# Performance work log

Hardware: AMD Instinct MI355X
Metric: run time of the kernel (lower is better)

## Reference

```python
import jax, jax.numpy as jnp
import numpy as np

N, E = 50000, 800000
IN_DIM, HID, HEADS, OUT_DIM = 128, 64, 4, 40
NEG_SLOPE = 0.2


def setup_inputs() -> dict:
    key = jax.random.key(0)
    ks = jax.random.split(key, 12)
    x = jax.random.normal(ks[0], (N, IN_DIM), dtype=jnp.float32)
    edge_index = jax.random.randint(ks[1], (2, E), 0, N, dtype=jnp.int64)
    timesteps = jax.random.randint(ks[2], (N,), 0, 100, dtype=jnp.int64)
    s = 1.0 / np.sqrt(IN_DIM)
    W_proj = jax.random.uniform(ks[3], (IN_DIM, HID), jnp.float32, -s, s)
    b_proj = jnp.zeros((HID,), jnp.float32)
    time_emb = jax.random.normal(ks[4], (100, HID), dtype=jnp.float32)
    sg = 1.0 / np.sqrt(HID)
    W_gat = jax.random.uniform(ks[5], (HID, HEADS * HID), jnp.float32, -sg, sg)
    att_src = jax.random.uniform(ks[6], (HEADS, HID), jnp.float32, -sg, sg)
    att_dst = jax.random.uniform(ks[7], (HEADS, HID), jnp.float32, -sg, sg)
    b_gat = jnp.zeros((HEADS * HID,), jnp.float32)
    sc = 1.0 / np.sqrt(HEADS * HID)
    W_cls = jax.random.uniform(ks[8], (HEADS * HID, OUT_DIM), jnp.float32, -sc, sc)
    b_cls = jnp.zeros((OUT_DIM,), jnp.float32)
    return {"x": x, "edge_index": edge_index, "timesteps": timesteps,
            "W_proj": W_proj, "b_proj": b_proj, "time_emb": time_emb,
            "W_gat": W_gat, "att_src": att_src, "att_dst": att_dst, "b_gat": b_gat,
            "W_cls": W_cls, "b_cls": b_cls}


def reference(x, edge_index, timesteps, W_proj, b_proj, time_emb,
              W_gat, att_src, att_dst, b_gat, W_cls, b_cls):
    n = x.shape[0]
    # feature projection + ReLU + time embedding
    h0 = jax.nn.relu(x @ W_proj + b_proj) + time_emb[timesteps]  # [N, HID]
    # --- GATConv (PyG semantics, add_self_loops=True, concat heads) ---
    h = (h0 @ W_gat).reshape(n, HEADS, HID)              # [N, H, C]
    a_src = jnp.einsum('nhc,hc->nh', h, att_src)         # [N, H]
    a_dst = jnp.einsum('nhc,hc->nh', h, att_dst)
    loops = jnp.arange(n, dtype=edge_index.dtype)
    src = jnp.concatenate([edge_index[0], loops])        # [E+N]
    dst = jnp.concatenate([edge_index[1], loops])
    e = jax.nn.leaky_relu(a_src[src] + a_dst[dst], NEG_SLOPE)  # [E+N, H]
    # segment softmax over incoming edges per destination node
    m = jax.ops.segment_max(e, dst, num_segments=n)      # [N, H]
    p = jnp.exp(e - m[dst])
    denom = jax.ops.segment_sum(p, dst, num_segments=n)  # [N, H]
    alpha = p / (denom[dst] + 1e-16)                     # [E+N, H]
    msg = alpha[:, :, None] * h[src]                     # [E+N, H, C]
    agg = jax.ops.segment_sum(msg, dst, num_segments=n)  # [N, H, C]
    gat_out = agg.reshape(n, HEADS * HID) + b_gat
    # ReLU + (dropout is identity in eval) + classifier
    return jax.nn.relu(gat_out) @ W_cls + b_cls          # [N, OUT_DIM]
```

## Files before the change

kernel.cpp:

```cpp
#include <hip/hip_runtime.h>
#include <hip/hip_fp16.h>

#define IN_DIM 128
#define HID 64
#define HEADS 4
#define OUT_DIM 40
#define CAP 64
#define NEG 0.2f
#define PA_EPB 4096
#define BKT_SH 9
#define BKT_CAP 10240
#define GPAD 264
#define HGP 72

__device__ __forceinline__ float lrelu(float v) { return v > 0.f ? v : NEG * v; }

union HU { float2 f2; __half2 h2[2]; };
union HU2 { float4 f4; __half2 h2[4]; };

typedef _Float16 f16x8 __attribute__((ext_vector_type(8)));
typedef float f32x4 __attribute__((ext_vector_type(4)));
union FU { float4 f4; f16x8 v; };

__global__ __launch_bounds__(256) void partA_kernel(
    const int* __restrict__ ei, int E, int nbkt, int paBlocks,
    int* __restrict__ cnt, unsigned int* __restrict__ ebuf,
    const float* __restrict__ Wg, const float* __restrict__ attS,
    const float* __restrict__ attD, const float* __restrict__ Wc,
    const float* __restrict__ Wp,
    float* __restrict__ aSf, float* __restrict__ aDf,
    __half* __restrict__ WgT, __half* __restrict__ WcTg,
    __half* __restrict__ WpT, __half* __restrict__ BsdT)
{
    if (blockIdx.x >= paBlocks) {
        int gid = (blockIdx.x - paBlocks) * 256 + threadIdx.x;
        if (gid < 256) {
            int k = gid >> 2, hd = gid & 3;
            const float* wr = Wg + k * 256 + hd * 64;
            const float* as = attS + hd * 64;
            const float* ad = attD + hd * 64;
            float ss = 0.f, dd = 0.f;
            for (int c = 0; c < 64; ++c) { float w = wr[c]; ss += w * as[c]; dd += w * ad[c]; }
            aSf[k * 4 + hd] = ss;
            aDf[k * 4 + hd] = dd;
        } else if (gid < 256 + 256 * HID) {
            int i = gid - 256;
            int o = i >> 6, k = i & 63;
            WgT[i] = __float2half(Wg[k * 256 + o]);
        } else if (gid < 256 + 256 * HID + OUT_DIM * 256) {
            int i = gid - 256 - 256 * HID;
            int o = i >> 8, k = i & 255;
            WcTg[i] = __float2half(Wc[k * OUT_DIM + o]);
        } else if (gid < 26880 + HID * IN_DIM) {
            int i = gid - 26880;
            int o = i >> 7, k = i & 127;
            WpT[i] = __float2half(Wp[k * HID + o]);
        } else if (gid < 26880 + HID * IN_DIM + 16 * HID) {
            int i = gid - 26880 - HID * IN_DIM;
            int n2 = i >> 6, k = i & 63;
            float v = 0.f;
            if (n2 < 8) {
                int hd = n2 & 3;
                const float* wr = Wg + k * 256 + hd * 64;
                const float* av = (n2 < 4) ? (attS + hd * 64) : (attD + hd * 64);
                for (int c = 0; c < 64; ++c) v += wr[c] * av[c];
            }
            BsdT[i] = __float2half(v);
        }
        return;
    }

    __shared__ int localCnt[128];
    __shared__ int baseArr[128];
    for (int i = threadIdx.x; i < nbkt; i += 256) localCnt[i] = 0;
    __syncthreads();

    const int e0 = blockIdx.x * PA_EPB + threadIdx.x;
    unsigned short l[16];
#pragma unroll
    for (int j = 0; j < 16; ++j) {
        int e = e0 + j * 256;
        if (e < E) {
            int d = ei[E + e];
            l[j] = (unsigned short)atomicAdd(&localCnt[d >> BKT_SH], 1);
        }
    }
    __syncthreads();
    for (int i = threadIdx.x; i < nbkt; i += 256)
        baseArr[i] = atomicAdd(&cnt[i], localCnt[i]);
    __syncthreads();
#pragma unroll
    for (int j = 0; j < 16; ++j) {
        int e = e0 + j * 256;
        if (e < E) {
            int s = ei[e];
            int d = ei[E + e];
            int b = d >> BKT_SH;
            int off = baseArr[b] + (int)l[j];
            if (off < BKT_CAP)
                ebuf[(size_t)b * BKT_CAP + off] =
                    ((unsigned)(d & ((1 << BKT_SH) - 1)) << 16) | (unsigned)s;
        }
    }
}

__global__ __launch_bounds__(256) void partBproj_kernel(
    const unsigned int* __restrict__ ebuf, const int* __restrict__ cnt,
    int* __restrict__ deg, unsigned short* __restrict__ csr, int nbkt,
    const float* __restrict__ x, const __half* __restrict__ WpT,
    const float* __restrict__ bp, const float* __restrict__ temb,
    const int* __restrict__ ts, const __half* __restrict__ BsdT,
    __half* __restrict__ h0h, float* __restrict__ aS, float* __restrict__ aD, int N)
{
    __shared__ __align__(16) char smem[32 * HGP * 2];

    if ((int)blockIdx.x < nbkt) {
        int* cntL = (int*)smem;
        const int b = blockIdx.x;
        for (int i = threadIdx.x; i < 512; i += 256) cntL[i] = 0;
        __syncthreads();

        int cb = cnt[b]; cb = cb < BKT_CAP ? cb : BKT_CAP;
        const unsigned int* eb = ebuf + (size_t)b * BKT_CAP;
        const int d0 = b << BKT_SH;
        for (int i = threadIdx.x; i < cb; i += 256) {
            unsigned v = eb[i];
            int dloc = v >> 16;
            int slot = atomicAdd(&cntL[dloc], 1);
            if (slot < CAP)
                csr[((size_t)(d0 + dloc) << 6) + slot] = (unsigned short)(v & 0xFFFFu);
        }
        __syncthreads();
        for (int i = threadIdx.x; i < 512; i += 256) {
            int d = d0 + i;
            if (d < N) deg[d] = cntL[i];
        }
        return;
    }

    __half* h0L = (__half*)smem;
    const int t = threadIdx.x;
    const int lane = t & 63, wq = t >> 6;
    const int m16 = lane & 15, quad = lane >> 4;
    const int mt = wq >> 1;
    const int ntb = (wq & 1) * 2;
    const int nodeBase = ((int)blockIdx.x - nbkt) * 32;

    f32x4 acc[2];
    acc[0] = (f32x4){0.f, 0.f, 0.f, 0.f};
    acc[1] = (f32x4){0.f, 0.f, 0.f, 0.f};

    {
        int n = nodeBase + mt * 16 + m16; n = n < N ? n : N - 1;
        const float* xr = x + (size_t)n * IN_DIM;
#pragma unroll
        for (int ks = 0; ks < 4; ++ks) {
            float4 xa = *(const float4*)(xr + ks * 32 + quad * 8);
            float4 xb = *(const float4*)(xr + ks * 32 + quad * 8 + 4);
            HU2 u;
            u.h2[0] = __floats2half2_rn(xa.x, xa.y);
            u.h2[1] = __floats2half2_rn(xa.z, xa.w);
            u.h2[2] = __floats2half2_rn(xb.x, xb.y);
            u.h2[3] = __floats2half2_rn(xb.z, xb.w);
            FU a; a.f4 = u.f4;
#pragma unroll
            for (int q = 0; q < 2; ++q) {
                int o = (ntb + q) * 16 + m16;
                FU b; b.f4 = *(const float4*)(WpT + o * IN_DIM + ks * 32 + quad * 8);
                acc[q] = __builtin_amdgcn_mfma_f32_16x16x32_f16(a.v, b.v, acc[q], 0, 0, 0);
            }
        }
    }

    {
        float bv[2];
#pragma unroll
        for (int q = 0; q < 2; ++q) bv[q] = bp[(ntb + q) * 16 + m16];
#pragma unroll
        for (int r = 0; r < 4; ++r) {
            int nloc = mt * 16 + quad * 4 + r;
            int n = nodeBase + nloc;
            if (n < N) {
                int tv = ts[n];
                const float* te = temb + (size_t)tv * HID;
#pragma unroll
                for (int q = 0; q < 2; ++q) {
                    int c = (ntb + q) * 16 + m16;
                    float v = fmaxf(acc[q][r] + bv[q], 0.f) + te[c];
                    h0L[nloc * HGP + c] = __float2half(v);
                }
            }
        }
    }
    __syncthreads();

    {
        int row = t >> 3, ch = (t & 7) * 8;
        int n = nodeBase + row;
        if (n < N)
            *(float4*)(h0h + (size_t)n * HID + ch) = *(const float4*)(h0L + row * HGP + ch);
    }

    if (wq < 2) {
        f32x4 acc2 = (f32x4){0.f, 0.f, 0.f, 0.f};
#pragma unroll
        for (int ks = 0; ks < 2; ++ks) {
            FU a; a.f4 = *(const float4*)(h0L + (wq * 16 + m16) * HGP + ks * 32 + quad * 8);
            FU b; b.f4 = *(const float4*)(BsdT + m16 * 64 + ks * 32 + quad * 8);
            acc2 = __builtin_amdgcn_mfma_f32_16x16x32_f16(a.v, b.v, acc2, 0, 0, 0);
        }
#pragma unroll
        for (int r = 0; r < 4; ++r) {
            int n = nodeBase + wq * 16 + quad * 4 + r;
            if (n < N) {
                if (m16 < 4)      aS[n * 4 + m16]       = acc2[r];
                else if (m16 < 8) aD[n * 4 + (m16 - 4)] = acc2[r];
            }
        }
    }
}

__global__ __launch_bounds__(256) void agg_kernel(
    const __half* __restrict__ h0h, const float* __restrict__ aS,
    const float* __restrict__ aD, const int* __restrict__ deg,
    const unsigned short* __restrict__ csr, __half* __restrict__ agg0h, int N)
{
    __shared__ float p_lds[4 * CAP * HEADS];
    __shared__ int   s_lds[4 * CAP];

    const int t = threadIdx.x;
    const int lane = t & 63, wq = t >> 6;
    const int n = blockIdx.x * 4 + wq;
    if (n >= N) return;
    const int hd16 = lane >> 4, li = lane & 15;

    const float adn = aD[n * 4 + hd16];
    const float es = lrelu(aS[n * 4 + hd16] + adn);

    int dn = deg[n]; dn = dn < CAP ? dn : CAP;
    const unsigned short* cs = csr + (size_t)n * CAP;
    float* pL = p_lds + wq * CAP * HEADS;
    int*   sL = s_lds + wq * CAP;

    float m = -1e30f;
    for (int i = li; i < dn; i += 16) {
        int src = cs[i];
        if (hd16 == 0) sL[i] = src << 7;
        float e = lrelu(aS[src * 4 + hd16] + adn);
        pL[i * HEADS + hd16] = e;
        m = fmaxf(m, e);
    }
#pragma unroll
    for (int off = 8; off > 0; off >>= 1)
        m = fmaxf(m, __shfl_xor(m, off));
    m = fmaxf(m, es);
    float mh[4], esh[4];
#pragma unroll
    for (int h = 0; h < 4; ++h) {
        mh[h]  = __shfl(m, h * 16);
        esh[h] = __shfl(es, h * 16);
    }

    float sp = 0.f;
    for (int idx = lane; idx < dn * 4; idx += 64) {
        float p = __expf(pL[idx] - mh[idx & 3]);
        pL[idx] = p;
        sp += p;
    }
#pragma unroll
    for (int off = 4; off < 64; off <<= 1)
        sp += __shfl_xor(sp, off);
    float pselfh[4], invh[4];
#pragma unroll
    for (int h = 0; h < 4; ++h) {
        float sh = __shfl(sp, h);
        pselfh[h] = __expf(esh[h] - mh[h]);
        invh[h] = 1.f / (sh + pselfh[h] + 1e-16f);
    }

    const int half = lane >> 5;
    const int ch2 = lane & 31;
    const char* hb = (const char*)h0h;
    const int laneByte = ch2 << 2;

    float2 acc[4];
    {
        float lo = 0.f, hi = 0.f;
        if (half == 0) {
            __half2 v2 = *(const __half2*)(hb + ((size_t)n << 7) + laneByte);
            float2 f = __half22float2(v2);
            lo = f.x; hi = f.y;
        }
#pragma unroll
        for (int h = 0; h < 4; ++h) {
            acc[h].x = pselfh[h] * lo;
            acc[h].y = pselfh[h] * hi;
        }
    }
    int i = 0;
    for (; i + 8 <= dn; i += 8) {
        int off0 = sL[i + 0 + half];
        int off1 = sL[i + 2 + half];
        int off2 = sL[i + 4 + half];
        int off3 = sL[i + 6 + half];
        __half2 v0 = *(const __half2*)(hb + off0 + laneByte);
        __half2 v1 = *(const __half2*)(hb + off1 + laneByte);
        __half2 v2 = *(const __half2*)(hb + off2 + laneByte);
        __half2 v3 = *(const __half2*)(hb + off3 + laneByte);
        float4 p0 = *(const float4*)(pL + (i + 0 + half) * 4);
        float4 p1 = *(const float4*)(pL + (i + 2 + half) * 4);
        float4 p2 = *(const float4*)(pL + (i + 4 + half) * 4);
        float4 p3 = *(const float4*)(pL + (i + 6 + half) * 4);
        float2 f;
        f = __half22float2(v0);
        acc[0].x += p0.x * f.x; acc[0].y += p0.x * f.y;
        acc[1].x += p0.y * f.x; acc[1].y += p0.y * f.y;
        acc[2].x += p0.z * f.x; acc[2].y += p0.z * f.y;
        acc[3].x += p0.w * f.x; acc[3].y += p0.w * f.y;
        f = __half22float2(v1);
        acc[0].x += p1.x * f.x; acc[0].y += p1.x * f.y;
        acc[1].x += p1.y * f.x; acc[1].y += p1.y * f.y;
        acc[2].x += p1.z * f.x; acc[2].y += p1.z * f.y;
        acc[3].x += p1.w * f.x; acc[3].y += p1.w * f.y;
        f = __half22float2(v2);
        acc[0].x += p2.x * f.x; acc[0].y += p2.x * f.y;
        acc[1].x += p2.y * f.x; acc[1].y += p2.y * f.y;
        acc[2].x += p2.z * f.x; acc[2].y += p2.z * f.y;
        acc[3].x += p2.w * f.x; acc[3].y += p2.w * f.y;
        f = __half22float2(v3);
        acc[0].x += p3.x * f.x; acc[0].y += p3.x * f.y;
        acc[1].x += p3.y * f.x; acc[1].y += p3.y * f.y;
        acc[2].x += p3.z * f.x; acc[2].y += p3.z * f.y;
        acc[3].x += p3.w * f.x; acc[3].y += p3.w * f.y;
    }
    for (; i + 2 <= dn; i += 2) {
        int off0 = sL[i + half];
        __half2 v0 = *(const __half2*)(hb + off0 + laneByte);
        float4 p0 = *(const float4*)(pL + (i + half) * 4);
        float2 f = __half22float2(v0);
        acc[0].x += p0.x * f.x; acc[0].y += p0.x * f.y;
        acc[1].x += p0.y * f.x; acc[1].y += p0.y * f.y;
        acc[2].x += p0.z * f.x; acc[2].y += p0.z * f.y;
        acc[3].x += p0.w * f.x; acc[3].y += p0.w * f.y;
    }
    if (i < dn && half == 0) {
        int off0 = sL[i];
        __half2 v0 = *(const __half2*)(hb + off0 + laneByte);
        float4 p0 = *(const float4*)(pL + i * 4);
        float2 f = __half22float2(v0);
        acc[0].x += p0.x * f.x; acc[0].y += p0.x * f.y;
        acc[1].x += p0.y * f.x; acc[1].y += p0.y * f.y;
        acc[2].x += p0.z * f.x; acc[2].y += p0.z * f.y;
        acc[3].x += p0.w * f.x; acc[3].y += p0.w * f.y;
    }
#pragma unroll
    for (int h = 0; h < 4; ++h) {
        acc[h].x += __shfl_xor(acc[h].x, 32);
        acc[h].y += __shfl_xor(acc[h].y, 32);
    }
    if (lane < 32) {
        __half2* dst = (__half2*)(agg0h + (size_t)n * 256);
#pragma unroll
        for (int h = 0; h < 4; ++h)
            dst[h * 32 + ch2] = __floats2half2_rn(acc[h].x * invh[h],
                                                  acc[h].y * invh[h]);
    }
}

__global__ __launch_bounds__(256) void gatcls_kernel(
    const __half* __restrict__ agg0h, const __half* __restrict__ WgT,
    const float* __restrict__ bg, const __half* __restrict__ WcTg,
    const float* __restrict__ bc, float* __restrict__ out, int N)
{
    __shared__ __half gtile[32 * GPAD];

    const int t = threadIdx.x;
    const int lane = t & 63, wq = t >> 6;
    const int m16 = lane & 15, quad = lane >> 4;
    const int nodeBase = blockIdx.x * 32;

    {
        const int h = wq;
        f32x4 acc[2][4];
#pragma unroll
        for (int mt = 0; mt < 2; ++mt)
#pragma unroll
            for (int nt = 0; nt < 4; ++nt)
                acc[mt][nt] = (f32x4){0.f, 0.f, 0.f, 0.f};

#pragma unroll
        for (int ks = 0; ks < 2; ++ks) {
            FU a[2], b[4];
#pragma unroll
            for (int mt = 0; mt < 2; ++mt) {
                int n = nodeBase + mt * 16 + m16; n = n < N ? n : N - 1;
                a[mt].f4 = *(const float4*)(agg0h + (size_t)n * 256 + h * 64 + ks * 32 + quad * 8);
            }
#pragma unroll
            for (int nt = 0; nt < 4; ++nt) {
                int o = h * 64 + nt * 16 + m16;
                b[nt].f4 = *(const float4*)(WgT + o * 64 + ks * 32 + quad * 8);
            }
#pragma unroll
            for (int mt = 0; mt < 2; ++mt)
#pragma unroll
                for (int nt = 0; nt < 4; ++nt)
                    acc[mt][nt] = __builtin_amdgcn_mfma_f32_16x16x32_f16(
                        a[mt].v, b[nt].v, acc[mt][nt], 0, 0, 0);
        }
#pragma unroll
        for (int nt = 0; nt < 4; ++nt) {
            int o = h * 64 + nt * 16 + m16;
            float bv = bg[o];
#pragma unroll
            for (int mt = 0; mt < 2; ++mt) {
#pragma unroll
                for (int r = 0; r < 4; ++r) {
                    int nloc = mt * 16 + quad * 4 + r;
                    gtile[nloc * GPAD + o] = __float2half(fmaxf(acc[mt][nt][r] + bv, 0.f));
                }
            }
        }
    }
    __syncthreads();

    {
        const int mt = wq >> 1;
        const int ntCount = (wq & 1) ? 1 : 2;
        const int ntBase = (wq & 1) ? 2 : 0;
        f32x4 acc2[2];
        acc2[0] = (f32x4){0.f, 0.f, 0.f, 0.f};
        acc2[1] = (f32x4){0.f, 0.f, 0.f, 0.f};
#pragma unroll
        for (int ks = 0; ks < 8; ++ks) {
            FU a; a.f4 = *(const float4*)(gtile + (mt * 16 + m16) * GPAD + ks * 32 + quad * 8);
            for (int q = 0; q < ntCount; ++q) {
                int o = (ntBase + q) * 16 + m16;
                int oc = o < OUT_DIM ? o : OUT_DIM - 1;
                FU b; b.f4 = *(const float4*)(WcTg + oc * 256 + ks * 32 + quad * 8);
                acc2[q] = __builtin_amdgcn_mfma_f32_16x16x32_f16(a.v, b.v, acc2[q], 0, 0, 0);
            }
        }
        for (int q = 0; q < ntCount; ++q) {
            int o = (ntBase + q) * 16 + m16;
            if (o < OUT_DIM) {
                float bv = bc[o];
#pragma unroll
                for (int r = 0; r < 4; ++r) {
                    int n = nodeBase + mt * 16 + quad * 4 + r;
                    if (n < N) out[(size_t)n * OUT_DIM + o] = acc2[q][r] + bv;
                }
            }
        }
    }
}

extern "C" void kernel_launch(void* const* d_in, const int* in_sizes, int n_in,
                              void* d_out, int out_size, void* d_ws, size_t ws_size,
                              hipStream_t stream) {
    const float* x    = (const float*)d_in[0];
    const int*   ei   = (const int*)d_in[1];
    const int*   ts   = (const int*)d_in[2];
    const float* Wp   = (const float*)d_in[3];
    const float* bp   = (const float*)d_in[4];
    const float* temb = (const float*)d_in[5];
    const float* Wg   = (const float*)d_in[6];
    const float* attS = (const float*)d_in[7];
    const float* attD = (const float*)d_in[8];
    const float* bg   = (const float*)d_in[9];
    const float* Wc   = (const float*)d_in[10];
    const float* bc   = (const float*)d_in[11];
    float* out = (float*)d_out;

    const int N = in_sizes[0] / IN_DIM;
    const int E = in_sizes[1] / 2;
    const int nbkt = (N + (1 << BKT_SH) - 1) >> BKT_SH;

    char* w = (char*)d_ws;
    __half*         h0h   = (__half*)w;         w += (size_t)N * HID * 2;
    __half*         agg0h = (__half*)w;         w += (size_t)N * 256 * 2;
    float*          aS    = (float*)w;          w += (size_t)N * HEADS * 4;
    float*          aD    = (float*)w;          w += (size_t)N * HEADS * 4;
    int*            deg   = (int*)w;            w += (size_t)N * 4;
    unsigned short* csr   = (unsigned short*)w; w += (size_t)N * CAP * 2;
    unsigned int*   ebuf  = (unsigned int*)w;   w += (size_t)nbkt * BKT_CAP * 4;
    int*            cnt   = (int*)w;            w += (size_t)nbkt * 4;
    float*          aSf   = (float*)w;          w += 256 * 4;
    float*          aDf   = (float*)w;          w += 256 * 4;
    __half*         WgT   = (__half*)w;         w += (size_t)256 * HID * 2;
    __half*         WcTg  = (__half*)w;         w += (size_t)OUT_DIM * 256 * 2;
    __half*         WpT   = (__half*)w;         w += (size_t)HID * IN_DIM * 2;
    __half*         BsdT  = (__half*)w;         w += (size_t)16 * HID * 2;

    const int paBlocks = (E + PA_EPB - 1) / PA_EPB;
    const int prepWork = 256 + 256 * HID + OUT_DIM * 256
                       + HID * IN_DIM + 16 * HID;
    const int prepBlocks = (prepWork + 255) / 256;
    const int projBlocks = (N + 31) / 32;

    hipMemsetAsync(cnt, 0, (size_t)nbkt * 4, stream);
    partA_kernel<<<paBlocks + prepBlocks, 256, 0, stream>>>(
        ei, E, nbkt, paBlocks, cnt, ebuf, Wg, attS, attD, Wc, Wp,
        aSf, aDf, WgT, WcTg, WpT, BsdT);
    partBproj_kernel<<<nbkt + projBlocks, 256, 0, stream>>>(
        ebuf, cnt, deg, csr, nbkt, x, WpT, bp, temb, ts, BsdT, h0h, aS, aD, N);
    agg_kernel<<<(N + 3) / 4, 256, 0, stream>>>(h0h, aS, aD, deg, csr, agg0h, N);
    gatcls_kernel<<<(N + 31) / 32, 256, 0, stream>>>(agg0h, WgT, bg, WcTg, bc, out, N);
}
```

Measured before the change: 198.6 us.

## Replace two-pass bucketed CSR build with direct global-atomic scatter

The two-level bucket sort (partA bucketing into ebuf, then per-bucket shared-memory slotting) is replaced by one pass in which each edge does a global atomicAdd on deg[dst] and writes its source straight into the fixed-capacity CSR row. Degree zeroing moves into the weight-prep kernel, which removes the memset and the unused aSf/aDf computation, and the CSR build now runs in the same launch as the projection. This drops one full read/write of the edge buffer and a launch, but uses many scattered global atomics on random destinations in place of shared-memory atomics.

```diff
diff --git a/kernel.cpp b/kernel.cpp
--- a/kernel.cpp
+++ b/kernel.cpp
@@ -7,9 +7,6 @@
 #define OUT_DIM 40
 #define CAP 64
 #define NEG 0.2f
-#define PA_EPB 4096
-#define BKT_SH 9
-#define BKT_CAP 10240
 #define GPAD 264
 #define HGP 72
 
@@ -22,129 +19,71 @@
 typedef float f32x4 __attribute__((ext_vector_type(4)));
 union FU { float4 f4; f16x8 v; };
 
-__global__ __launch_bounds__(256) void partA_kernel(
-    const int* __restrict__ ei, int E, int nbkt, int paBlocks,
-    int* __restrict__ cnt, unsigned int* __restrict__ ebuf,
+__global__ __launch_bounds__(256) void prep_kernel(
     const float* __restrict__ Wg, const float* __restrict__ attS,
     const float* __restrict__ attD, const float* __restrict__ Wc,
     const float* __restrict__ Wp,
-    float* __restrict__ aSf, float* __restrict__ aDf,
     __half* __restrict__ WgT, __half* __restrict__ WcTg,
-    __half* __restrict__ WpT, __half* __restrict__ BsdT)
+    __half* __restrict__ WpT, __half* __restrict__ BsdT,
+    int* __restrict__ deg, int N)
 {
-    if (blockIdx.x >= paBlocks) {
-        int gid = (blockIdx.x - paBlocks) * 256 + threadIdx.x;
-        if (gid < 256) {
-            int k = gid >> 2, hd = gid & 3;
+    int gid = blockIdx.x * 256 + threadIdx.x;
+    if (gid < 16384) {
+        int o = gid >> 6, k = gid & 63;
+        WgT[gid] = __float2half(Wg[k * 256 + o]);
+    } else if (gid < 26624) {
+        int i = gid - 16384;
+        int o = i >> 8, k = i & 255;
+        WcTg[i] = __float2half(Wc[k * OUT_DIM + o]);
+    } else if (gid < 34816) {
+        int i = gid - 26624;
+        int o = i >> 7, k = i & 127;
+        WpT[i] = __float2half(Wp[k * HID + o]);
+    } else if (gid < 35840) {
+        int i = gid - 34816;
+        int n2 = i >> 6, k = i & 63;
+        float v = 0.f;
+        if (n2 < 8) {
+            int hd = n2 & 3;
             const float* wr = Wg + k * 256 + hd * 64;
-            const float* as = attS + hd * 64;
-            const float* ad = attD + hd * 64;
-            float ss = 0.f, dd = 0.f;
-            for (int c = 0; c < 64; ++c) { float w = wr[c]; ss += w * as[c]; dd += w * ad[c]; }
-            aSf[k * 4 + hd] = ss;
-            aDf[k * 4 + hd] = dd;
-        } else if (gid < 256 + 256 * HID) {
-            int i = gid - 256;
-            int o = i >> 6, k = i & 63;
-            WgT[i] = __float2half(Wg[k * 256 + o]);
-        } else if (gid < 256 + 256 * HID + OUT_DIM * 256) {
-            int i = gid - 256 - 256 * HID;
-            int o = i >> 8, k = i & 255;
-            WcTg[i] = __float2half(Wc[k * OUT_DIM + o]);
-        } else if (gid < 26880 + HID * IN_DIM) {
-            int i = gid - 26880;
-            int o = i >> 7, k = i & 127;
-            WpT[i] = __float2half(Wp[k * HID + o]);
-        } else if (gid < 26880 + HID * IN_DIM + 16 * HID) {
-            int i = gid - 26880 - HID * IN_DIM;
-            int n2 = i >> 6, k = i & 63;
-            float v = 0.f;
-            if (n2 < 8) {
-                int hd = n2 & 3;
-                const float* wr = Wg + k * 256 + hd * 64;
-                const float* av = (n2 < 4) ? (attS + hd * 64) : (attD + hd * 64);
-                for (int c = 0; c < 64; ++c) v += wr[c] * av[c];
-            }
-            BsdT[i] = __float2half(v);
-        }
-        return;
-    }
-
-    __shared__ int localCnt[128];
-    __shared__ int baseArr[128];
-    for (int i = threadIdx.x; i < nbkt; i += 256) localCnt[i] = 0;
-    __syncthreads();
-
-    const int e0 = blockIdx.x * PA_EPB + threadIdx.x;
-    unsigned short l[16];
-#pragma unroll
-    for (int j = 0; j < 16; ++j) {
-        int e = e0 + j * 256;
-        if (e < E) {
-            int d = ei[E + e];
-            l[j] = (unsigned short)atomicAdd(&localCnt[d >> BKT_SH], 1);
-        }
-    }
-    __syncthreads();
-    for (int i = threadIdx.x; i < nbkt; i += 256)
-        baseArr[i] = atomicAdd(&cnt[i], localCnt[i]);
-    __syncthreads();
-#pragma unroll
-    for (int j = 0; j < 16; ++j) {
-        int e = e0 + j * 256;
-        if (e < E) {
-            int s = ei[e];
-            int d = ei[E + e];
-            int b = d >> BKT_SH;
-            int off = baseArr[b] + (int)l[j];
-            if (off < BKT_CAP)
-                ebuf[(size_t)b * BKT_CAP + off] =
-                    ((unsigned)(d & ((1 << BKT_SH) - 1)) << 16) | (unsigned)s;
-        }
+            const float* av = (n2 < 4) ? (attS + hd * 64) : (attD + hd * 64);
+            for (int c = 0; c < 64; ++c) v += wr[c] * av[c];
+        }
+        BsdT[i] = __float2half(v);
+    } else {
+        int d = gid - 35840;
+        if (d < N) deg[d] = 0;
     }
 }
 
-__global__ __launch_bounds__(256) void partBproj_kernel(
-    const unsigned int* __restrict__ ebuf, const int* __restrict__ cnt,
-    int* __restrict__ deg, unsigned short* __restrict__ csr, int nbkt,
+__global__ __launch_bounds__(256) void binproj_kernel(
+    const int* __restrict__ ei, int E, int nbin,
+    int* __restrict__ deg, unsigned short* __restrict__ csr,
     const float* __restrict__ x, const __half* __restrict__ WpT,
     const float* __restrict__ bp, const float* __restrict__ temb,
     const int* __restrict__ ts, const __half* __restrict__ BsdT,
     __half* __restrict__ h0h, float* __restrict__ aS, float* __restrict__ aD, int N)
 {
-    __shared__ __align__(16) char smem[32 * HGP * 2];
-
-    if ((int)blockIdx.x < nbkt) {
-        int* cntL = (int*)smem;
-        const int b = blockIdx.x;
-        for (int i = threadIdx.x; i < 512; i += 256) cntL[i] = 0;
-        __syncthreads();
-
-        int cb = cnt[b]; cb = cb < BKT_CAP ? cb : BKT_CAP;
-        const unsigned int* eb = ebuf + (size_t)b * BKT_CAP;
-        const int d0 = b << BKT_SH;
-        for (int i = threadIdx.x; i < cb; i += 256) {
-            unsigned v = eb[i];
-            int dloc = v >> 16;
-            int slot = atomicAdd(&cntL[dloc], 1);
+    __shared__ __align__(16) __half h0L[32 * HGP];
+
+    if ((int)blockIdx.x < nbin) {
+        int e = blockIdx.x * 256 + threadIdx.x;
+        if (e < E) {
+            int s = ei[e];
+            int d = ei[E + e];
+            int slot = atomicAdd(&deg[d], 1);
             if (slot < CAP)
-                csr[((size_t)(d0 + dloc) << 6) + slot] = (unsigned short)(v & 0xFFFFu);
-        }
-        __syncthreads();
-        for (int i = threadIdx.x; i < 512; i += 256) {
-            int d = d0 + i;
-            if (d < N) deg[d] = cntL[i];
+                csr[(size_t)d * CAP + slot] = (unsigned short)s;
         }
         return;
     }
 
-    __half* h0L = (__half*)smem;
     const int t = threadIdx.x;
     const int lane = t & 63, wq = t >> 6;
     const int m16 = lane & 15, quad = lane >> 4;
     const int mt = wq >> 1;
     const int ntb = (wq & 1) * 2;
-    const int nodeBase = ((int)blockIdx.x - nbkt) * 32;
+    const int nodeBase = ((int)blockIdx.x - nbin) * 32;
 
     f32x4 acc[2];
     acc[0] = (f32x4){0.f, 0.f, 0.f, 0.f};
@@ -474,7 +413,6 @@
 
     const int N = in_sizes[0] / IN_DIM;
     const int E = in_sizes[1] / 2;
-    const int nbkt = (N + (1 << BKT_SH) - 1) >> BKT_SH;
 
     char* w = (char*)d_ws;
     __half*         h0h   = (__half*)w;         w += (size_t)N * HID * 2;
@@ -483,27 +421,20 @@
     float*          aD    = (float*)w;          w += (size_t)N * HEADS * 4;
     int*            deg   = (int*)w;            w += (size_t)N * 4;
     unsigned short* csr   = (unsigned short*)w; w += (size_t)N * CAP * 2;
-    unsigned int*   ebuf  = (unsigned int*)w;   w += (size_t)nbkt * BKT_CAP * 4;
-    int*            cnt   = (int*)w;            w += (size_t)nbkt * 4;
-    float*          aSf   = (float*)w;          w += 256 * 4;
-    float*          aDf   = (float*)w;          w += 256 * 4;
     __half*         WgT   = (__half*)w;         w += (size_t)256 * HID * 2;
     __half*         WcTg  = (__half*)w;         w += (size_t)OUT_DIM * 256 * 2;
     __half*         WpT   = (__half*)w;         w += (size_t)HID * IN_DIM * 2;
     __half*         BsdT  = (__half*)w;         w += (size_t)16 * HID * 2;
 
-    const int paBlocks = (E + PA_EPB - 1) / PA_EPB;
-    const int prepWork = 256 + 256 * HID + OUT_DIM * 256
-                       + HID * IN_DIM + 16 * HID;
+    const int prepWork  = 35840 + N;
     const int prepBlocks = (prepWork + 255) / 256;
+    const int nbin      = (E + 255) / 256;
     const int projBlocks = (N + 31) / 32;
 
-    hipMemsetAsync(cnt, 0, (size_t)nbkt * 4, stream);
-    partA_kernel<<<paBlocks + prepBlocks, 256, 0, stream>>>(
-        ei, E, nbkt, paBlocks, cnt, ebuf, Wg, attS, attD, Wc, Wp,
-        aSf, aDf, WgT, WcTg, WpT, BsdT);
-    partBproj_kernel<<<nbkt + projBlocks, 256, 0, stream>>>(
-        ebuf, cnt, deg, csr, nbkt, x, WpT, bp, temb, ts, BsdT, h0h, aS, aD, N);
+    prep_kernel<<<prepBlocks, 256, 0, stream>>>(
+        Wg, attS, attD, Wc, Wp, WgT, WcTg, WpT, BsdT, deg, N);
+    binproj_kernel<<<nbin + projBlocks, 256, 0, stream>>>(
+        ei, E, nbin, deg, csr, x, WpT, bp, temb, ts, BsdT, h0h, aS, aD, N);
     agg_kernel<<<(N + 3) / 4, 256, 0, stream>>>(h0h, aS, aD, deg, csr, agg0h, N);
     gatcls_kernel<<<(N + 31) / 32, 256, 0, stream>>>(agg0h, WgT, bg, WcTg, bc, out, N);
 }
```

New measurement: 217.6 us. 1.1x slower.

## Fuse attention aggregation with GAT linear and classifier into one kernel

Applied to the files above, without the earlier changes.

Merges the aggregation kernel with the GAT-projection and classifier MFMA kernel. The per-node aggregated features now stay in LDS instead of making a round trip through a global fp16 buffer. Each 4-node block runs 16-row MFMA tiles with only 4 valid rows and reloads the full WgT and WcTg weights per block, which adds wasted matrix work and weight traffic. It also drops the unused aSf/aDf precompute and shrinks edges per partition block from 4096 to 1024 to launch more blocks.

```diff
diff --git a/kernel.cpp b/kernel.cpp
--- a/kernel.cpp
+++ b/kernel.cpp
@@ -7,10 +7,10 @@
 #define OUT_DIM 40
 #define CAP 64
 #define NEG 0.2f
-#define PA_EPB 4096
+#define PA_EPB 1024
 #define BKT_SH 9
 #define BKT_CAP 10240
-#define GPAD 264
+#define GP2 264
 #define HGP 72
 
 __device__ __forceinline__ float lrelu(float v) { return v > 0.f ? v : NEG * v; }
@@ -28,35 +28,24 @@
     const float* __restrict__ Wg, const float* __restrict__ attS,
     const float* __restrict__ attD, const float* __restrict__ Wc,
     const float* __restrict__ Wp,
-    float* __restrict__ aSf, float* __restrict__ aDf,
     __half* __restrict__ WgT, __half* __restrict__ WcTg,
     __half* __restrict__ WpT, __half* __restrict__ BsdT)
 {
     if (blockIdx.x >= paBlocks) {
         int gid = (blockIdx.x - paBlocks) * 256 + threadIdx.x;
-        if (gid < 256) {
-            int k = gid >> 2, hd = gid & 3;
-            const float* wr = Wg + k * 256 + hd * 64;
-            const float* as = attS + hd * 64;
-            const float* ad = attD + hd * 64;
-            float ss = 0.f, dd = 0.f;
-            for (int c = 0; c < 64; ++c) { float w = wr[c]; ss += w * as[c]; dd += w * ad[c]; }
-            aSf[k * 4 + hd] = ss;
-            aDf[k * 4 + hd] = dd;
-        } else if (gid < 256 + 256 * HID) {
-            int i = gid - 256;
-            int o = i >> 6, k = i & 63;
-            WgT[i] = __float2half(Wg[k * 256 + o]);
-        } else if (gid < 256 + 256 * HID + OUT_DIM * 256) {
-            int i = gid - 256 - 256 * HID;
+        if (gid < 16384) {
+            int o = gid >> 6, k = gid & 63;
+            WgT[gid] = __float2half(Wg[k * 256 + o]);
+        } else if (gid < 26624) {
+            int i = gid - 16384;
             int o = i >> 8, k = i & 255;
             WcTg[i] = __float2half(Wc[k * OUT_DIM + o]);
-        } else if (gid < 26880 + HID * IN_DIM) {
-            int i = gid - 26880;
+        } else if (gid < 34816) {
+            int i = gid - 26624;
             int o = i >> 7, k = i & 127;
             WpT[i] = __float2half(Wp[k * HID + o]);
-        } else if (gid < 26880 + HID * IN_DIM + 16 * HID) {
-            int i = gid - 26880 - HID * IN_DIM;
+        } else if (gid < 35840) {
+            int i = gid - 34816;
             int n2 = i >> 6, k = i & 63;
             float v = 0.f;
             if (n2 < 8) {
@@ -76,9 +65,9 @@
     __syncthreads();
 
     const int e0 = blockIdx.x * PA_EPB + threadIdx.x;
-    unsigned short l[16];
-#pragma unroll
-    for (int j = 0; j < 16; ++j) {
+    unsigned short l[4];
+#pragma unroll
+    for (int j = 0; j < 4; ++j) {
         int e = e0 + j * 256;
         if (e < E) {
             int d = ei[E + e];
@@ -90,7 +79,7 @@
         baseArr[i] = atomicAdd(&cnt[i], localCnt[i]);
     __syncthreads();
 #pragma unroll
-    for (int j = 0; j < 16; ++j) {
+    for (int j = 0; j < 4; ++j) {
         int e = e0 + j * 256;
         if (e < E) {
             int s = ei[e];
@@ -220,236 +209,206 @@
     }
 }
 
-__global__ __launch_bounds__(256) void agg_kernel(
+__global__ __launch_bounds__(256) void aggcls_kernel(
     const __half* __restrict__ h0h, const float* __restrict__ aS,
     const float* __restrict__ aD, const int* __restrict__ deg,
-    const unsigned short* __restrict__ csr, __half* __restrict__ agg0h, int N)
+    const unsigned short* __restrict__ csr,
+    const __half* __restrict__ WgT, const float* __restrict__ bg,
+    const __half* __restrict__ WcTg, const float* __restrict__ bc,
+    float* __restrict__ out, int N)
 {
-    __shared__ float p_lds[4 * CAP * HEADS];
-    __shared__ int   s_lds[4 * CAP];
+    __shared__ __half agg0L[16 * GP2];
+    __shared__ union {
+        struct { float p[4 * CAP * HEADS]; int s[4 * CAP]; } g;
+        __half gatL[16 * GP2];
+    } su;
 
     const int t = threadIdx.x;
     const int lane = t & 63, wq = t >> 6;
     const int n = blockIdx.x * 4 + wq;
-    if (n >= N) return;
     const int hd16 = lane >> 4, li = lane & 15;
-
-    const float adn = aD[n * 4 + hd16];
-    const float es = lrelu(aS[n * 4 + hd16] + adn);
-
-    int dn = deg[n]; dn = dn < CAP ? dn : CAP;
-    const unsigned short* cs = csr + (size_t)n * CAP;
-    float* pL = p_lds + wq * CAP * HEADS;
-    int*   sL = s_lds + wq * CAP;
-
-    float m = -1e30f;
-    for (int i = li; i < dn; i += 16) {
-        int src = cs[i];
-        if (hd16 == 0) sL[i] = src << 7;
-        float e = lrelu(aS[src * 4 + hd16] + adn);
-        pL[i * HEADS + hd16] = e;
-        m = fmaxf(m, e);
-    }
-#pragma unroll
-    for (int off = 8; off > 0; off >>= 1)
-        m = fmaxf(m, __shfl_xor(m, off));
-    m = fmaxf(m, es);
-    float mh[4], esh[4];
-#pragma unroll
-    for (int h = 0; h < 4; ++h) {
-        mh[h]  = __shfl(m, h * 16);
-        esh[h] = __shfl(es, h * 16);
-    }
-
-    float sp = 0.f;
-    for (int idx = lane; idx < dn * 4; idx += 64) {
-        float p = __expf(pL[idx] - mh[idx & 3]);
-        pL[idx] = p;
-        sp += p;
-    }
-#pragma unroll
-    for (int off = 4; off < 64; off <<= 1)
-        sp += __shfl_xor(sp, off);
-    float pselfh[4], invh[4];
-#pragma unroll
-    for (int h = 0; h < 4; ++h) {
-        float sh = __shfl(sp, h);
-        pselfh[h] = __expf(esh[h] - mh[h]);
-        invh[h] = 1.f / (sh + pselfh[h] + 1e-16f);
-    }
-
     const int half = lane >> 5;
     const int ch2 = lane & 31;
     const char* hb = (const char*)h0h;
     const int laneByte = ch2 << 2;
 
-    float2 acc[4];
-    {
-        float lo = 0.f, hi = 0.f;
-        if (half == 0) {
-            __half2 v2 = *(const __half2*)(hb + ((size_t)n << 7) + laneByte);
-            float2 f = __half22float2(v2);
-            lo = f.x; hi = f.y;
-        }
+    if (n < N) {
+        const float adn = aD[n * 4 + hd16];
+        const float es = lrelu(aS[n * 4 + hd16] + adn);
+
+        int dn = deg[n]; dn = dn < CAP ? dn : CAP;
+        const unsigned short* cs = csr + (size_t)n * CAP;
+        float* pL = su.g.p + wq * CAP * HEADS;
+        int*   sL = su.g.s + wq * CAP;
+
+        float m = -1e30f;
+        for (int i = li; i < dn; i += 16) {
+            int src = cs[i];
+            if (hd16 == 0) sL[i] = src << 7;
+            float e = lrelu(aS[src * 4 + hd16] + adn);
+            pL[i * HEADS + hd16] = e;
+            m = fmaxf(m, e);
+        }
+#pragma unroll
+        for (int off = 8; off > 0; off >>= 1)
+            m = fmaxf(m, __shfl_xor(m, off));
+        m = fmaxf(m, es);
+        float mh[4], esh[4];
 #pragma unroll
         for (int h = 0; h < 4; ++h) {
-            acc[h].x = pselfh[h] * lo;
-            acc[h].y = pselfh[h] * hi;
-        }
-    }
-    int i = 0;
-    for (; i + 8 <= dn; i += 8) {
-        int off0 = sL[i + 0 + half];
-        int off1 = sL[i + 2 + half];
-        int off2 = sL[i + 4 + half];
-        int off3 = sL[i + 6 + half];
-        __half2 v0 = *(const __half2*)(hb + off0 + laneByte);
-        __half2 v1 = *(const __half2*)(hb + off1 + laneByte);
-        __half2 v2 = *(const __half2*)(hb + off2 + laneByte);
-        __half2 v3 = *(const __half2*)(hb + off3 + laneByte);
-        float4 p0 = *(const float4*)(pL + (i + 0 + half) * 4);
-        float4 p1 = *(const float4*)(pL + (i + 2 + half) * 4);
-        float4 p2 = *(const float4*)(pL + (i + 4 + half) * 4);
-        float4 p3 = *(const float4*)(pL + (i + 6 + half) * 4);
-        float2 f;
-        f = __half22float2(v0);
-        acc[0].x += p0.x * f.x; acc[0].y += p0.x * f.y;
-        acc[1].x += p0.y * f.x; acc[1].y += p0.y * f.y;
-        acc[2].x += p0.z * f.x; acc[2].y += p0.z * f.y;
-        acc[3].x += p0.w * f.x; acc[3].y += p0.w * f.y;
-        f = __half22float2(v1);
-        acc[0].x += p1.x * f.x; acc[0].y += p1.x * f.y;
-        acc[1].x += p1.y * f.x; acc[1].y += p1.y * f.y;
-        acc[2].x += p1.z * f.x; acc[2].y += p1.z * f.y;
-        acc[3].x += p1.w * f.x; acc[3].y += p1.w * f.y;
-        f = __half22float2(v2);
-        acc[0].x += p2.x * f.x; acc[0].y += p2.x * f.y;
-        acc[1].x += p2.y * f.x; acc[1].y += p2.y * f.y;
-        acc[2].x += p2.z * f.x; acc[2].y += p2.z * f.y;
-        acc[3].x += p2.w * f.x; acc[3].y += p2.w * f.y;
-        f = __half22float2(v3);
-        acc[0].x += p3.x * f.x; acc[0].y += p3.x * f.y;
-        acc[1].x += p3.y * f.x; acc[1].y += p3.y * f.y;
-        acc[2].x += p3.z * f.x; acc[2].y += p3.z * f.y;
-        acc[3].x += p3.w * f.x; acc[3].y += p3.w * f.y;
-    }
-    for (; i + 2 <= dn; i += 2) {
-        int off0 = sL[i + half];
-        __half2 v0 = *(const __half2*)(hb + off0 + laneByte);
-        float4 p0 = *(const float4*)(pL + (i + half) * 4);
-        float2 f = __half22float2(v0);
-        acc[0].x += p0.x * f.x; acc[0].y += p0.x * f.y;
-        acc[1].x += p0.y * f.x; acc[1].y += p0.y * f.y;
-        acc[2].x += p0.z * f.x; acc[2].y += p0.z * f.y;
-        acc[3].x += p0.w * f.x; acc[3].y += p0.w * f.y;
-    }
-    if (i < dn && half == 0) {
-        int off0 = sL[i];
-        __half2 v0 = *(const __half2*)(hb + off0 + laneByte);
-        float4 p0 = *(const float4*)(pL + i * 4);
-        float2 f = __half22float2(v0);
-        acc[0].x += p0.x * f.x; acc[0].y += p0.x * f.y;
-        acc[1].x += p0.y * f.x; acc[1].y += p0.y * f.y;
-        acc[2].x += p0.z * f.x; acc[2].y += p0.z * f.y;
-        acc[3].x += p0.w * f.x; acc[3].y += p0.w * f.y;
-    }
-#pragma unroll
-    for (int h = 0; h < 4; ++h) {
-        acc[h].x += __shfl_xor(acc[h].x, 32);
-        acc[h].y += __shfl_xor(acc[h].y, 32);
-    }
-    if (lane < 32) {
-        __half2* dst = (__half2*)(agg0h + (size_t)n * 256);
-#pragma unroll
-        for (int h = 0; h < 4; ++h)
-            dst[h * 32 + ch2] = __floats2half2_rn(acc[h].x * invh[h],
-                                                  acc[h].y * invh[h]);
-    }
-}
-
-__global__ __launch_bounds__(256) void gatcls_kernel(
-    const __half* __restrict__ agg0h, const __half* __restrict__ WgT,
-    const float* __restrict__ bg, const __half* __restrict__ WcTg,
-    const float* __restrict__ bc, float* __restrict__ out, int N)
-{
-    __shared__ __half gtile[32 * GPAD];
-
-    const int t = threadIdx.x;
-    const int lane = t & 63, wq = t >> 6;
+            mh[h]  = __shfl(m, h * 16);
+            esh[h] = __shfl(es, h * 16);
+        }
+
+        float sp = 0.f;
+        for (int idx = lane; idx < dn * 4; idx += 64) {
+            float p = __expf(pL[idx] - mh[idx & 3]);
+            pL[idx] = p;
+            sp += p;
+        }
+#pragma unroll
+        for (int off = 4; off < 64; off <<= 1)
+            sp += __shfl_xor(sp, off);
+        float pselfh[4], invh[4];
+#pragma unroll
+        for (int h = 0; h < 4; ++h) {
+            float sh = __shfl(sp, h);
+            pselfh[h] = __expf(esh[h] - mh[h]);
+            invh[h] = 1.f / (sh + pselfh[h] + 1e-16f);
+        }
+
+        float2 acc[4];
+        {
+            float lo = 0.f, hi = 0.f;
+            if (half == 0) {
+                __half2 v2 = *(const __half2*)(hb + ((size_t)n << 7) + laneByte);
+                float2 f = __half22float2(v2);
+                lo = f.x; hi = f.y;
+            }
+#pragma unroll
+            for (int h = 0; h < 4; ++h) {
+                acc[h].x = pselfh[h] * lo;
+                acc[h].y = pselfh[h] * hi;
+            }
+        }
+        int i = 0;
+        for (; i + 8 <= dn; i += 8) {
+            int off0 = sL[i + 0 + half];
+            int off1 = sL[i + 2 + half];
+            int off2 = sL[i + 4 + half];
+            int off3 = sL[i + 6 + half];
+            __half2 v0 = *(const __half2*)(hb + off0 + laneByte);
+            __half2 v1 = *(const __half2*)(hb + off1 + laneByte);
+            __half2 v2 = *(const __half2*)(hb + off2 + laneByte);
+            __half2 v3 = *(const __half2*)(hb + off3 + laneByte);
+            float4 p0 = *(const float4*)(pL + (i + 0 + half) * 4);
+            float4 p1 = *(const float4*)(pL + (i + 2 + half) * 4);
+            float4 p2 = *(const float4*)(pL + (i + 4 + half) * 4);
+            float4 p3 = *(const float4*)(pL + (i + 6 + half) * 4);
+            float2 f;
+            f = __half22float2(v0);
+            acc[0].x += p0.x * f.x; acc[0].y += p0.x * f.y;
+            acc[1].x += p0.y * f.x; acc[1].y += p0.y * f.y;
+            acc[2].x += p0.z * f.x; acc[2].y += p0.z * f.y;
+            acc[3].x += p0.w * f.x; acc[3].y += p0.w * f.y;
+            f = __half22float2(v1);
+            acc[0].x += p1.x * f.x; acc[0].y += p1.x * f.y;
+            acc[1].x += p1.y * f.x; acc[1].y += p1.y * f.y;
+            acc[2].x += p1.z * f.x; acc[2].y += p1.z * f.y;
+            acc[3].x += p1.w * f.x; acc[3].y += p1.w * f.y;
+            f = __half22float2(v2);
+            acc[0].x += p2.x * f.x; acc[0].y += p2.x * f.y;
+            acc[1].x += p2.y * f.x; acc[1].y += p2.y * f.y;
+            acc[2].x += p2.z * f.x; acc[2].y += p2.z * f.y;
+            acc[3].x += p2.w * f.x; acc[3].y += p2.w * f.y;
+            f = __half22float2(v3);
+            acc[0].x += p3.x * f.x; acc[0].y += p3.x * f.y;
+            acc[1].x += p3.y * f.x; acc[1].y += p3.y * f.y;
+            acc[2].x += p3.z * f.x; acc[2].y += p3.z * f.y;
+            acc[3].x += p3.w * f.x; acc[3].y += p3.w * f.y;
+        }
+        for (; i + 2 <= dn; i += 2) {
+            int off0 = sL[i + half];
+            __half2 v0 = *(const __half2*)(hb + off0 + laneByte);
+            float4 p0 = *(const float4*)(pL + (i + half) * 4);
+            float2 f = __half22float2(v0);
+            acc[0].x += p0.x * f.x; acc[0].y += p0.x * f.y;
+            acc[1].x += p0.y * f.x; acc[1].y += p0.y * f.y;
+            acc[2].x += p0.z * f.x; acc[2].y += p0.z * f.y;
+            acc[3].x += p0.w * f.x; acc[3].y += p0.w * f.y;
+        }
+        if (i < dn && half == 0) {
+            int off0 = sL[i];
+            __half2 v0 = *(const __half2*)(hb + off0 + laneByte);
+            float4 p0 = *(const float4*)(pL + i * 4);
+            float2 f = __half22float2(v0);
+            acc[0].x += p0.x * f.x; acc[0].y += p0.x * f.y;
+            acc[1].x += p0.y * f.x; acc[1].y += p0.y * f.y;
+            acc[2].x += p0.z * f.x; acc[2].y += p0.z * f.y;
+            acc[3].x += p0.w * f.x; acc[3].y += p0.w * f.y;
+        }
+#pragma unroll
+        for (int h = 0; h < 4; ++h) {
+            acc[h].x += __shfl_xor(acc[h].x, 32);
+            acc[h].y += __shfl_xor(acc[h].y, 32);
+        }
+        if (lane < 32) {
+            __half2* dst = (__half2*)(agg0L + wq * GP2);
+#pragma unroll
+            for (int h = 0; h < 4; ++h)
+                dst[h * 32 + ch2] = __floats2half2_rn(acc[h].x * invh[h],
+                                                      acc[h].y * invh[h]);
+        }
+    }
+    __syncthreads();
+
     const int m16 = lane & 15, quad = lane >> 4;
-    const int nodeBase = blockIdx.x * 32;
 
     {
         const int h = wq;
-        f32x4 acc[2][4];
-#pragma unroll
-        for (int mt = 0; mt < 2; ++mt)
-#pragma unroll
-            for (int nt = 0; nt < 4; ++nt)
-                acc[mt][nt] = (f32x4){0.f, 0.f, 0.f, 0.f};
-
+        f32x4 acc1[4];
+#pragma unroll
+        for (int nt = 0; nt < 4; ++nt)
+            acc1[nt] = (f32x4){0.f, 0.f, 0.f, 0.f};
 #pragma unroll
         for (int ks = 0; ks < 2; ++ks) {
-            FU a[2], b[4];
-#pragma unroll
-            for (int mt = 0; mt < 2; ++mt) {
-                int n = nodeBase + mt * 16 + m16; n = n < N ? n : N - 1;
-                a[mt].f4 = *(const float4*)(agg0h + (size_t)n * 256 + h * 64 + ks * 32 + quad * 8);
-            }
+            FU a; a.f4 = *(const float4*)(agg0L + m16 * GP2 + h * 64 + ks * 32 + quad * 8);
 #pragma unroll
             for (int nt = 0; nt < 4; ++nt) {
                 int o = h * 64 + nt * 16 + m16;
-                b[nt].f4 = *(const float4*)(WgT + o * 64 + ks * 32 + quad * 8);
-            }
-#pragma unroll
-            for (int mt = 0; mt < 2; ++mt)
-#pragma unroll
-                for (int nt = 0; nt < 4; ++nt)
-                    acc[mt][nt] = __builtin_amdgcn_mfma_f32_16x16x32_f16(
-                        a[mt].v, b[nt].v, acc[mt][nt], 0, 0, 0);
+                FU b; b.f4 = *(const float4*)(WgT + o * 64 + ks * 32 + quad * 8);
+                acc1[nt] = __builtin_amdgcn_mfma_f32_16x16x32_f16(a.v, b.v, acc1[nt], 0, 0, 0);
+            }
         }
 #pragma unroll
         for (int nt = 0; nt < 4; ++nt) {
             int o = h * 64 + nt * 16 + m16;
             float bv = bg[o];
 #pragma unroll
-            for (int mt = 0; mt < 2; ++mt) {
-#pragma unroll
-                for (int r = 0; r < 4; ++r) {
-                    int nloc = mt * 16 + quad * 4 + r;
-                    gtile[nloc * GPAD + o] = __float2half(fmaxf(acc[mt][nt][r] + bv, 0.f));
-                }
-            }
-        }
-    }
-    __syncthreads();
-
-    {
-        const int mt = wq >> 1;
-        const int ntCount = (wq & 1) ? 1 : 2;
-        const int ntBase = (wq & 1) ? 2 : 0;
-        f32x4 acc2[2];
-        acc2[0] = (f32x4){0.f, 0.f, 0.f, 0.f};
-        acc2[1] = (f32x4){0.f, 0.f, 0.f, 0.f};
+            for (int r = 0; r < 4; ++r) {
+                int row = quad * 4 + r;
+                su.gatL[row * GP2 + o] = __float2half(fmaxf(acc1[nt][r] + bv, 0.f));
+            }
+        }
+    }
+    __syncthreads();
+
+    if (wq < 3) {
+        f32x4 acc2 = (f32x4){0.f, 0.f, 0.f, 0.f};
+        int o = wq * 16 + m16;
+        int oc = o < OUT_DIM ? o : OUT_DIM - 1;
 #pragma unroll
         for (int ks = 0; ks < 8; ++ks) {
-            FU a; a.f4 = *(const float4*)(gtile + (mt * 16 + m16) * GPAD + ks * 32 + quad * 8);
-            for (int q = 0; q < ntCount; ++q) {
-                int o = (ntBase + q) * 16 + m16;
-                int oc = o < OUT_DIM ? o : OUT_DIM - 1;
-                FU b; b.f4 = *(const float4*)(WcTg + oc * 256 + ks * 32 + quad * 8);
-                acc2[q] = __builtin_amdgcn_mfma_f32_16x16x32_f16(a.v, b.v, acc2[q], 0, 0, 0);
-            }
-        }
-        for (int q = 0; q < ntCount; ++q) {
-            int o = (ntBase + q) * 16 + m16;
-            if (o < OUT_DIM) {
-                float bv = bc[o];
-#pragma unroll
-                for (int r = 0; r < 4; ++r) {
-                    int n = nodeBase + mt * 16 + quad * 4 + r;
-                    if (n < N) out[(size_t)n * OUT_DIM + o] = acc2[q][r] + bv;
-                }
+            FU a; a.f4 = *(const float4*)(su.gatL + m16 * GP2 + ks * 32 + quad * 8);
+            FU b; b.f4 = *(const float4*)(WcTg + oc * 256 + ks * 32 + quad * 8);
+            acc2 = __builtin_amdgcn_mfma_f32_16x16x32_f16(a.v, b.v, acc2, 0, 0, 0);
+        }
+        if (o < OUT_DIM && quad == 0) {
+            float bv = bc[o];
+#pragma unroll
+            for (int r = 0; r < 4; ++r) {
+                int nn = blockIdx.x * 4 + r;
+                if (nn < N) out[(size_t)nn * OUT_DIM + o] = acc2[r] + bv;
             }
         }
     }
@@ -478,32 +437,28 @@
 
     char* w = (char*)d_ws;
     __half*         h0h   = (__half*)w;         w += (size_t)N * HID * 2;
-    __half*         agg0h = (__half*)w;         w += (size_t)N * 256 * 2;
     float*          aS    = (float*)w;          w += (size_t)N * HEADS * 4;
     float*          aD    = (float*)w;          w += (size_t)N * HEADS * 4;
     int*            deg   = (int*)w;            w += (size_t)N * 4;
     unsigned short* csr   = (unsigned short*)w; w += (size_t)N * CAP * 2;
     unsigned int*   ebuf  = (unsigned int*)w;   w += (size_t)nbkt * BKT_CAP * 4;
     int*            cnt   = (int*)w;            w += (size_t)nbkt * 4;
-    float*          aSf   = (float*)w;          w += 256 * 4;
-    float*          aDf   = (float*)w;          w += 256 * 4;
     __half*         WgT   = (__half*)w;         w += (size_t)256 * HID * 2;
     __half*         WcTg  = (__half*)w;         w += (size_t)OUT_DIM * 256 * 2;
     __half*         WpT   = (__half*)w;         w += (size_t)HID * IN_DIM * 2;
     __half*         BsdT  = (__half*)w;         w += (size_t)16 * HID * 2;
 
-    const int paBlocks = (E + PA_EPB - 1) / PA_EPB;
-    const int prepWork = 256 + 256 * HID + OUT_DIM * 256
-                       + HID * IN_DIM + 16 * HID;
+    const int paBlocks  = (E + PA_EPB - 1) / PA_EPB;
+    const int prepWork  = 35840;
     const int prepBlocks = (prepWork + 255) / 256;
     const int projBlocks = (N + 31) / 32;
 
     hipMemsetAsync(cnt, 0, (size_t)nbkt * 4, stream);
     partA_kernel<<<paBlocks + prepBlocks, 256, 0, stream>>>(
         ei, E, nbkt, paBlocks, cnt, ebuf, Wg, attS, attD, Wc, Wp,
-        aSf, aDf, WgT, WcTg, WpT, BsdT);
+        WgT, WcTg, WpT, BsdT);
     partBproj_kernel<<<nbkt + projBlocks, 256, 0, stream>>>(
         ebuf, cnt, deg, csr, nbkt, x, WpT, bp, temb, ts, BsdT, h0h, aS, aD, N);
-    agg_kernel<<<(N + 3) / 4, 256, 0, stream>>>(h0h, aS, aD, deg, csr, agg0h, N);
-    gatcls_kernel<<<(N + 31) / 32, 256, 0, stream>>>(agg0h, WgT, bg, WcTg, bc, out, N);
+    aggcls_kernel<<<(N + 3) / 4, 256, 0, stream>>>(
+        h0h, aS, aD, deg, csr, WgT, bg, WcTg, bc, out, N);
 }
```

Result: slower. 253.4 us (+27.6%).
